# Performance work log

Measured on AMD Instinct MI355X. Metric: run time of the kernel, lower is better.

The kernel has to match this reference:

```python
import jax, jax.numpy as jnp
import numpy as np

N, E, H, G = 20000, 320000, 256, 128
FN, FE, OUT = 64, 16, 10
EPS_GEN = 1e-7
EPS_BN = 1e-5
EPS_IN = 1e-5


def _lstm_cell_c(x, W, b):
    # torch LSTMCell with zero (h0, c0); only cell state c' is used:
    # c' = sigmoid(i) * tanh(g).  W: [4H, F], gate order i, f, g, o.
    z = x @ W.T + b
    i, f, g, o = jnp.split(z, 4, axis=1)
    return jax.nn.sigmoid(i) * jnp.tanh(g)


def _segment_softmax(scores, seg, num):
    m = jax.ops.segment_max(scores, seg, num_segments=num)
    m = jnp.where(jnp.isfinite(m), m, 0.0)
    e = jnp.exp(scores - m[seg])
    s = jax.ops.segment_sum(e, seg, num_segments=num)
    return e / (s[seg] + 1e-16)


def _gen_conv(x, src, dst, edge_attr, t, w1, b1, gamma, beta, w2, b2):
    # GENConv (aggr='softmax', t learnable scalar, eps=1e-7, 2-layer MLP)
    msg = jax.nn.relu(x[src] + edge_attr) + EPS_GEN          # [E, H]
    alpha = _segment_softmax(msg * t, dst, N)                 # [E, H]
    aggr = jax.ops.segment_sum(alpha * msg, dst, num_segments=N)  # [N, H]
    h = x + aggr
    h = h @ w1.T + b1                                         # [N, 2H]
    # BatchNorm1d in eval mode (running_mean=0, running_var=1)
    h = h / jnp.sqrt(1.0 + EPS_BN) * gamma + beta
    h = jax.nn.relu(h)
    return h @ w2.T + b2                                      # [N, H]


def _instance_norm(x, batch):
    ones = jnp.ones((x.shape[0],), x.dtype)
    cnt = jnp.maximum(jax.ops.segment_sum(ones, batch, num_segments=G), 1.0)[:, None]
    mean = jax.ops.segment_sum(x, batch, num_segments=G) / cnt
    var = jax.ops.segment_sum(x * x, batch, num_segments=G) / cnt - mean ** 2
    return (x - mean[batch]) / jnp.sqrt(var[batch] + EPS_IN)


def setup_inputs() -> dict:
    key = jax.random.key(0)
    ks = jax.random.split(key, 24)

    def glorot(k, shape):
        lim = 1.0 / np.sqrt(shape[-1])
        return jax.random.uniform(k, shape, jnp.float32, -lim, lim)

    inp = {
        "x": jax.random.normal(ks[0], (N, FN), jnp.float32),
        "edge_index": jax.random.randint(ks[1], (2, E), 0, N),
        "edge_attr": jax.random.normal(ks[2], (E, FE), jnp.float32),
        "batch": jnp.sort(jax.random.randint(ks[3], (N,), 0, G)),
        # LSTMCell embeddings
        "node_W": glorot(ks[4], (4 * H, FN)),
        "node_b": glorot(ks[5], (4 * H,)),
        "edge_W": glorot(ks[6], (4 * H, FE)),
        "edge_b": glorot(ks[7], (4 * H,)),
        # GENConv 1
        "t1": jnp.float32(1.0),
        "g1_w1": glorot(ks[8], (2 * H, H)),
        "g1_b1": glorot(ks[9], (2 * H,)),
        "g1_gamma": jnp.ones((2 * H,), jnp.float32),
        "g1_beta": jnp.zeros((2 * H,), jnp.float32),
        "g1_w2": glorot(ks[10], (H, 2 * H)),
        "g1_b2": glorot(ks[11], (H,)),
        # GENConv 2
        "t2": jnp.float32(1.0),
        "g2_w1": glorot(ks[12], (2 * H, H)),
        "g2_b1": glorot(ks[13], (2 * H,)),
        "g2_gamma": jnp.ones((2 * H,), jnp.float32),
        "g2_beta": jnp.zeros((2 * H,), jnp.float32),
        "g2_w2": glorot(ks[14], (H, 2 * H)),
        "g2_b2": glorot(ks[15], (H,)),
        # output Linear
        "lin_w": glorot(ks[16], (OUT, H)),
        "lin_b": glorot(ks[17], (OUT,)),
    }
    return inp


def reference(x, edge_index, edge_attr, batch,
              node_W, node_b, edge_W, edge_b,
              t1, g1_w1, g1_b1, g1_gamma, g1_beta, g1_w2, g1_b2,
              t2, g2_w1, g2_b1, g2_gamma, g2_beta, g2_w2, g2_b2,
              lin_w, lin_b):
    src, dst = edge_index[0], edge_index[1]
    h = _lstm_cell_c(x, node_W, node_b)            # [N, H]
    ea = _lstm_cell_c(edge_attr, edge_W, edge_b)   # [E, H]
    h = jax.nn.relu(_gen_conv(h, src, dst, ea, t1, g1_w1, g1_b1, g1_gamma, g1_beta, g1_w2, g1_b2))
    h = _instance_norm(h, batch)
    h = jax.nn.relu(_gen_conv(h, src, dst, ea, t2, g2_w1, g2_b1, g2_gamma, g2_beta, g2_w2, g2_b2))
    h = _instance_norm(h, batch)
    pooled = jax.ops.segment_max(h, batch, num_segments=G)  # [G, H]
    pooled = jnp.where(jnp.isfinite(pooled), pooled, 0.0)
    # dropout is identity in eval mode
    out = pooled @ lin_w.T + lin_b
    return jax.nn.sigmoid(out)
```

## Files before the change

### kernel.cpp

```cpp
#include <hip/hip_runtime.h>
#include <math.h>

#define N_NODES 20000
#define N_EDGES 320000
#define HH      256
#define GG      128
#define FN      64
#define FE      16

__device__ __forceinline__ float fast_rcp(float x) {
    return __builtin_amdgcn_rcpf(x);
}
__device__ __forceinline__ float fast_sigmoid(float x) {
    return fast_rcp(1.f + __expf(-x));
}
__device__ __forceinline__ float sig_tanh(float zi, float zg) {
    float u = __expf(-zi);
    float v = __expf(2.f * zg);
    return (v - 1.f) * fast_rcp((1.f + u) * (v + 1.f));
}

__global__ void hist_k(const int* __restrict__ dst, int* __restrict__ cnt) {
    int e = blockIdx.x * blockDim.x + threadIdx.x;
    if (e < N_EDGES) atomicAdd(&cnt[dst[e]], 1);
}

__global__ __launch_bounds__(256) void scan1_k(const int* __restrict__ cnt,
                                               int* __restrict__ ex,
                                               int* __restrict__ bsum) {
    int b = blockIdx.x, t = threadIdx.x;
    int i = b * 256 + t;
    int v = (i < N_NODES) ? cnt[i] : 0;
    int lane = t & 63, w = t >> 6;
    int incl = v;
#pragma unroll
    for (int off = 1; off < 64; off <<= 1) {
        int u = __shfl_up(incl, off);
        if (lane >= off) incl += u;
    }
    __shared__ int wsum[4];
    if (lane == 63) wsum[w] = incl;
    __syncthreads();
    int woff = 0;
#pragma unroll
    for (int j = 0; j < 4; ++j)
        if (j < w) woff += wsum[j];
    if (i < N_NODES) ex[i] = woff + incl - v;
    if (t == 255) bsum[b] = woff + incl;
}

__global__ __launch_bounds__(128) void scan2_k(int* __restrict__ bsum, int nb) {
    int t = threadIdx.x;
    int v = (t < nb) ? bsum[t] : 0;
    int lane = t & 63, w = t >> 6;
    int incl = v;
#pragma unroll
    for (int off = 1; off < 64; off <<= 1) {
        int u = __shfl_up(incl, off);
        if (lane >= off) incl += u;
    }
    __shared__ int wsum[2];
    if (lane == 63) wsum[w] = incl;
    __syncthreads();
    int woff = (w == 1) ? wsum[0] : 0;
    if (t < nb) bsum[t] = woff + incl - v;
}

__global__ __launch_bounds__(256) void scan3_k(const int* __restrict__ cnt,
                                               const int* __restrict__ bsum,
                                               int* __restrict__ rowst,
                                               int* __restrict__ cursor) {
    int b = blockIdx.x, t = threadIdx.x;
    int i = b * 256 + t;
    if (i < N_NODES) {
        int v = rowst[i] + bsum[b];
        rowst[i] = v;
        cursor[i] = v;
        if (i == N_NODES - 1) rowst[N_NODES] = v + cnt[i];
    }
}

__global__ void scatter_k(const int* __restrict__ src,
                          const int* __restrict__ dst,
                          const float* __restrict__ eattr,
                          int* __restrict__ cursor, int* __restrict__ srcs,
                          float* __restrict__ eattrs) {
    int e = blockIdx.x * blockDim.x + threadIdx.x;
    if (e < N_EDGES) {
        int pos = atomicAdd(&cursor[dst[e]], 1);
        srcs[pos] = src[e];
        const float4* a = (const float4*)(eattr + (size_t)e * FE);
        float4* o = (float4*)(eattrs + (size_t)pos * FE);
        o[0] = a[0];
        o[1] = a[1];
        o[2] = a[2];
        o[3] = a[3];
    }
}

__global__ void repack_k(const float* __restrict__ W, const float* __restrict__ b,
                         float* __restrict__ W2, float* __restrict__ b2) {
    int idx = blockIdx.x * blockDim.x + threadIdx.x;
    if (idx < 512 * 64) {
        int r = idx >> 6, k = idx & 63;
        int c = r >> 1;
        int rs = (r & 1) ? (512 + c) : c;
        W2[idx] = W[rs * 64 + k];
    } else if (idx < 512 * 64 + 512) {
        int r = idx - 512 * 64;
        int c = r >> 1;
        int rs = (r & 1) ? (512 + c) : c;
        b2[r] = b[rs];
    }
}

#define NPB 8
__global__ __launch_bounds__(256, 4) void genconv_edge_k(
    const float* __restrict__ hin, const float* __restrict__ eattrs,
    const int* __restrict__ srcs, const int* __restrict__ rowst,
    const float* __restrict__ eW, const float* __restrict__ eb,
    const float* __restrict__ tptr, float* __restrict__ aout) {
    int tid = threadIdx.x;
    float wi[16], wg[16];
    const float4* Wi4 = (const float4*)(eW + (size_t)tid * FE);
    const float4* Wg4 = (const float4*)(eW + (size_t)(512 + tid) * FE);
#pragma unroll
    for (int q = 0; q < 4; ++q) {
        float4 a = Wi4[q], b = Wg4[q];
        wi[q * 4 + 0] = a.x; wi[q * 4 + 1] = a.y;
        wi[q * 4 + 2] = a.z; wi[q * 4 + 3] = a.w;
        wg[q * 4 + 0] = b.x; wg[q * 4 + 1] = b.y;
        wg[q * 4 + 2] = b.z; wg[q * 4 + 3] = b.w;
    }
    float bi = eb[tid], bg = eb[512 + tid];
    float tscale = tptr[0];
    int n0 = blockIdx.x * NPB;
    for (int u = 0; u < NPB; ++u) {
        int n = n0 + u;
        if (n >= N_NODES) break;
        int s0 = rowst[n], s1 = rowst[n + 1];
        float hself = hin[(size_t)n * HH + tid];
        float accE0 = 0.f, accWE0 = 0.f, accE1 = 0.f, accWE1 = 0.f;
        int j = s0;
        for (; j + 1 < s1; j += 2) {
            int sn0 = srcs[j], sn1 = srcs[j + 1];
            const float4* ap0 = (const float4*)(eattrs + (size_t)j * FE);
            const float4* ap1 = (const float4*)(eattrs + (size_t)(j + 1) * FE);
            float4 a0 = ap0[0], a1 = ap0[1], a2 = ap0[2], a3 = ap0[3];
            float4 c0 = ap1[0], c1 = ap1[1], c2 = ap1[2], c3 = ap1[3];
            float h0v = hin[(size_t)sn0 * HH + tid];
            float h1v = hin[(size_t)sn1 * HH + tid];
            float av[16] = {a0.x, a0.y, a0.z, a0.w, a1.x, a1.y, a1.z, a1.w,
                            a2.x, a2.y, a2.z, a2.w, a3.x, a3.y, a3.z, a3.w};
            float cv[16] = {c0.x, c0.y, c0.z, c0.w, c1.x, c1.y, c1.z, c1.w,
                            c2.x, c2.y, c2.z, c2.w, c3.x, c3.y, c3.z, c3.w};
            float zi0 = bi, zg0 = bg, zi1 = bi, zg1 = bg;
#pragma unroll
            for (int k = 0; k < FE; ++k) {
                zi0 += wi[k] * av[k];
                zg0 += wg[k] * av[k];
                zi1 += wi[k] * cv[k];
                zg1 += wg[k] * cv[k];
            }
            float ea0 = sig_tanh(zi0, zg0);
            float ea1 = sig_tanh(zi1, zg1);
            float m0 = fmaxf(h0v + ea0, 0.f) + 1e-7f;
            float m1 = fmaxf(h1v + ea1, 0.f) + 1e-7f;
            float p0 = __expf(tscale * m0);
            float p1 = __expf(tscale * m1);
            accE0 += p0;
            accWE0 += p0 * m0;
            accE1 += p1;
            accWE1 += p1 * m1;
        }
        if (j < s1) {
            int sn = srcs[j];
            const float4* ap = (const float4*)(eattrs + (size_t)j * FE);
            float4 a0 = ap[0], a1 = ap[1], a2 = ap[2], a3 = ap[3];
            float hv = hin[(size_t)sn * HH + tid];
            float av[16] = {a0.x, a0.y, a0.z, a0.w, a1.x, a1.y, a1.z, a1.w,
                            a2.x, a2.y, a2.z, a2.w, a3.x, a3.y, a3.z, a3.w};
            float zi = bi, zg = bg;
#pragma unroll
            for (int k = 0; k < FE; ++k) {
                zi += wi[k] * av[k];
                zg += wg[k] * av[k];
            }
            float eav = sig_tanh(zi, zg);
            float m0 = fmaxf(hv + eav, 0.f) + 1e-7f;
            float p0 = __expf(tscale * m0);
            accE0 += p0;
            accWE0 += p0 * m0;
        }
        float accE = accE0 + accE1, accWE = accWE0 + accWE1;
        aout[(size_t)n * HH + tid] = hself + accWE / (accE + 1e-16f);
    }
}

#define TM 128
#define TN 128
#define KB 16
__global__ __launch_bounds__(256, 2) void gemm_nt_k(
    const float* __restrict__ A, const float* __restrict__ B,
    const float* __restrict__ bias, const float* __restrict__ gamma,
    const float* __restrict__ beta, float* __restrict__ C, int M, int NN,
    int K, int mode) {
    __shared__ float As[KB][TM + 4];
    __shared__ float Bs[KB][TN + 4];
    int tid = threadIdx.x;
    int row0 = blockIdx.x * TM, col0 = blockIdx.y * TN;
    int tx = tid & 15, ty = tid >> 4;
    int lr = tid >> 2;
    int lc = (tid & 3) * 4;
    float4 va[2], vb[2];
#pragma unroll
    for (int h = 0; h < 2; ++h) {
        int r = lr + h * 64;
        int gr = row0 + r;
        va[h] = (gr < M) ? *(const float4*)&A[(size_t)gr * K + lc]
                         : make_float4(0.f, 0.f, 0.f, 0.f);
        vb[h] = *(const float4*)&B[(size_t)(col0 + r) * K + lc];
    }
    float acc[8][8] = {{0.f}};
    for (int k0 = 0; k0 < K; k0 += KB) {
#pragma unroll
        for (int h = 0; h < 2; ++h) {
            int r = lr + h * 64;
            As[lc + 0][r] = va[h].x;
            As[lc + 1][r] = va[h].y;
            As[lc + 2][r] = va[h].z;
            As[lc + 3][r] = va[h].w;
            Bs[lc + 0][r] = vb[h].x;
            Bs[lc + 1][r] = vb[h].y;
            Bs[lc + 2][r] = vb[h].z;
            Bs[lc + 3][r] = vb[h].w;
        }
        __syncthreads();
        int k1 = k0 + KB;
        if (k1 < K) {
#pragma unroll
            for (int h = 0; h < 2; ++h) {
                int r = lr + h * 64;
                int gr = row0 + r;
                va[h] = (gr < M)
                            ? *(const float4*)&A[(size_t)gr * K + k1 + lc]
                            : make_float4(0.f, 0.f, 0.f, 0.f);
                vb[h] = *(const float4*)&B[(size_t)(col0 + r) * K + k1 + lc];
            }
        }
#pragma unroll
        for (int k = 0; k < KB; ++k) {
            float4 a0 = *(const float4*)&As[k][ty * 4];
            float4 a1 = *(const float4*)&As[k][64 + ty * 4];
            float4 b0 = *(const float4*)&Bs[k][tx * 4];
            float4 b1 = *(const float4*)&Bs[k][64 + tx * 4];
            float av[8] = {a0.x, a0.y, a0.z, a0.w, a1.x, a1.y, a1.z, a1.w};
            float bv[8] = {b0.x, b0.y, b0.z, b0.w, b1.x, b1.y, b1.z, b1.w};
#pragma unroll
            for (int i = 0; i < 8; ++i)
#pragma unroll
                for (int j = 0; j < 8; ++j) acc[i][j] += av[i] * bv[j];
        }
        __syncthreads();
    }
    const float bn_rs = rsqrtf(1.f + 1e-5f);
#pragma unroll
    for (int gj = 0; gj < 2; ++gj) {
        int nb = col0 + gj * 64 + tx * 4;
        float bs[4], sc[4], sh[4];
#pragma unroll
        for (int j = 0; j < 4; ++j) {
            bs[j] = bias[nb + j];
            if (mode == 0) {
                sc[j] = gamma[nb + j] * bn_rs;
                sh[j] = beta[nb + j];
            }
        }
#pragma unroll
        for (int gi = 0; gi < 2; ++gi) {
#pragma unroll
            for (int i2 = 0; i2 < 4; ++i2) {
                int m = row0 + gi * 64 + ty * 4 + i2;
                if (m >= M) continue;
                int i = gi * 4 + i2;
                float y[4];
#pragma unroll
                for (int j = 0; j < 4; ++j) {
                    float v = acc[i][gj * 4 + j] + bs[j];
                    if (mode == 0) v = v * sc[j] + sh[j];
                    if (mode == 0 || mode == 1) v = fmaxf(v, 0.f);
                    y[j] = v;
                }
                if (mode == 3) {
                    float2 o;
                    o.x = sig_tanh(y[0], y[1]);
                    o.y = sig_tanh(y[2], y[3]);
                    *(float2*)&C[(size_t)m * (NN / 2) + nb / 2] = o;
                } else {
                    float4 o = {y[0], y[1], y[2], y[3]};
                    *(float4*)&C[(size_t)m * NN + nb] = o;
                }
            }
        }
    }
}

__device__ __forceinline__ int lowerb(const int* a, int n, int key) {
    int lo = 0, hi = n;
    while (lo < hi) {
        int mid = (lo + hi) >> 1;
        if (a[mid] < key) lo = mid + 1;
        else hi = mid;
    }
    return lo;
}

__global__ __launch_bounds__(256) void inst_norm_k(
    const float* __restrict__ x, const int* __restrict__ batch,
    float* __restrict__ y) {
    __shared__ int sS, sE;
    int g = blockIdx.x, t = threadIdx.x;
    if (t == 0) {
        sS = lowerb(batch, N_NODES, g);
        sE = lowerb(batch, N_NODES, g + 1);
    }
    __syncthreads();
    int s = sS, e = sE;
    float sum = 0.f, ss = 0.f;
    for (int n = s; n < e; ++n) {
        float v = x[(size_t)n * HH + t];
        sum += v;
        ss += v * v;
    }
    float c = (float)((e - s) > 0 ? (e - s) : 1);
    float mean = sum / c;
    float var = ss / c - mean * mean;
    float inv = rsqrtf(var + 1e-5f);
    for (int n = s; n < e; ++n) {
        float v = x[(size_t)n * HH + t];
        y[(size_t)n * HH + t] = (v - mean) * inv;
    }
}

__global__ __launch_bounds__(256) void inpool_k(
    const float* __restrict__ x, const int* __restrict__ batch,
    const float* __restrict__ lw, const float* __restrict__ lb,
    float* __restrict__ out) {
    __shared__ float pooled[HH];
    __shared__ int sS, sE;
    int g = blockIdx.x, t = threadIdx.x;
    if (t == 0) {
        sS = lowerb(batch, N_NODES, g);
        sE = lowerb(batch, N_NODES, g + 1);
    }
    __syncthreads();
    int s = sS, e = sE;
    float sum = 0.f, ss = 0.f;
    for (int n = s; n < e; ++n) {
        float v = x[(size_t)n * HH + t];
        sum += v;
        ss += v * v;
    }
    float c = (float)((e - s) > 0 ? (e - s) : 1);
    float mean = sum / c;
    float var = ss / c - mean * mean;
    float inv = rsqrtf(var + 1e-5f);
    float m = -3.0e38f;
    for (int n = s; n < e; ++n) {
        float v = (x[(size_t)n * HH + t] - mean) * inv;
        m = fmaxf(m, v);
    }
    pooled[t] = (e > s) ? m : 0.f;
    __syncthreads();
    if (t < 10) {
        float acc = lb[t];
        for (int k = 0; k < HH; ++k) acc += pooled[k] * lw[t * HH + k];
        out[g * 10 + t] = fast_sigmoid(acc);
    }
}

extern "C" void kernel_launch(void* const* d_in, const int* in_sizes, int n_in,
                              void* d_out, int out_size, void* d_ws,
                              size_t ws_size, hipStream_t stream) {
    const float* x      = (const float*)d_in[0];
    const int*   ei     = (const int*)d_in[1];
    const float* eattr  = (const float*)d_in[2];
    const int*   batch  = (const int*)d_in[3];
    const float* nodeW  = (const float*)d_in[4];
    const float* nodeb  = (const float*)d_in[5];
    const float* edgeW  = (const float*)d_in[6];
    const float* edgeb  = (const float*)d_in[7];
    const float* t1     = (const float*)d_in[8];
    const float* g1w1   = (const float*)d_in[9];
    const float* g1b1   = (const float*)d_in[10];
    const float* g1g    = (const float*)d_in[11];
    const float* g1be   = (const float*)d_in[12];
    const float* g1w2   = (const float*)d_in[13];
    const float* g1b2   = (const float*)d_in[14];
    const float* t2     = (const float*)d_in[15];
    const float* g2w1   = (const float*)d_in[16];
    const float* g2b1   = (const float*)d_in[17];
    const float* g2g    = (const float*)d_in[18];
    const float* g2be   = (const float*)d_in[19];
    const float* g2w2   = (const float*)d_in[20];
    const float* g2b2   = (const float*)d_in[21];
    const float* linw   = (const float*)d_in[22];
    const float* linb   = (const float*)d_in[23];
    float* out = (float*)d_out;

    const int* srcA = ei;
    const int* dstA = ei + N_EDGES;

    float* F0 = (float*)d_ws;
    float* F1 = F0 + (size_t)N_NODES * HH;
    float* F2 = F1 + (size_t)N_NODES * HH;
    float* W2 = F2 + (size_t)N_NODES * 2 * HH;
    float* b2 = W2 + 512 * 64;
    float* eattrs = b2 + 512;
    int* cnt    = (int*)(eattrs + (size_t)N_EDGES * FE);
    int* cursor = cnt + N_NODES;
    int* rowst  = cursor + N_NODES;
    int* srcs   = rowst + N_NODES + 1;
    int* bsum   = srcs + N_EDGES;

    const int NSCB = (N_NODES + 255) / 256;

    hipMemsetAsync(cnt, 0, N_NODES * sizeof(int), stream);
    hist_k<<<(N_EDGES + 255) / 256, 256, 0, stream>>>(dstA, cnt);
    scan1_k<<<NSCB, 256, 0, stream>>>(cnt, rowst, bsum);
    scan2_k<<<1, 128, 0, stream>>>(bsum, NSCB);
    scan3_k<<<NSCB, 256, 0, stream>>>(cnt, bsum, rowst, cursor);
    scatter_k<<<(N_EDGES + 255) / 256, 256, 0, stream>>>(srcA, dstA, eattr,
                                                         cursor, srcs, eattrs);

    repack_k<<<(512 * 64 + 512 + 255) / 256, 256, 0, stream>>>(nodeW, nodeb,
                                                               W2, b2);
    dim3 gemm_grid1((N_NODES + TM - 1) / TM, 512 / TN);
    dim3 gemm_grid2((N_NODES + TM - 1) / TM, 256 / TN);
    gemm_nt_k<<<gemm_grid1, 256, 0, stream>>>(x, W2, b2, nullptr, nullptr, F0,
                                              N_NODES, 512, 64, 3);

    genconv_edge_k<<<(N_NODES + NPB - 1) / NPB, 256, 0, stream>>>(
        F0, eattrs, srcs, rowst, edgeW, edgeb, t1, F1);
    gemm_nt_k<<<gemm_grid1, 256, 0, stream>>>(F1, g1w1, g1b1, g1g, g1be, F2,
                                              N_NODES, 512, 256, 0);
    gemm_nt_k<<<gemm_grid2, 256, 0, stream>>>(F2, g1w2, g1b2, nullptr, nullptr,
                                              F1, N_NODES, 256, 512, 1);
    inst_norm_k<<<GG, 256, 0, stream>>>(F1, batch, F0);

    genconv_edge_k<<<(N_NODES + NPB - 1) / NPB, 256, 0, stream>>>(
        F0, eattrs, srcs, rowst, edgeW, edgeb, t2, F1);
    gemm_nt_k<<<gemm_grid1, 256, 0, stream>>>(F1, g2w1, g2b1, g2g, g2be, F2,
                                              N_NODES, 512, 256, 0);
    gemm_nt_k<<<gemm_grid2, 256, 0, stream>>>(F2, g2w2, g2b2, nullptr, nullptr,
                                              F1, N_NODES, 256, 512, 1);

    inpool_k<<<GG, 256, 0, stream>>>(F1, batch, linw, linb, out);
}
```

Before: 985.6 us.

## Precompute edge LSTM embeddings once in bf16 via GEMM, reuse in both convs

The edge LSTM embedding was recomputed inside each genconv edge kernel, a 16-wide dot product plus sig_tanh per edge per channel, and done twice. It is now materialized once by the tiled GEMM with a new bf16-output epilogue, and both conv passes read it in CSR order. This trades compute for memory traffic: a 320000x256 bf16 tensor (~164MB) is written once and read twice instead of 64B of edge attributes per edge. Dropping the weight registers also lets launch bounds rise to 8 blocks per SM, and bf16 storage adds rounding error to the edge embedding.

```diff
diff --git a/kernel.cpp b/kernel.cpp
--- a/kernel.cpp
+++ b/kernel.cpp
@@ -1,4 +1,5 @@
 #include <hip/hip_runtime.h>
+#include <hip/hip_bf16.h>
 #include <math.h>
 
 #define N_NODES 20000
@@ -99,15 +100,15 @@
 }
 
 __global__ void repack_k(const float* __restrict__ W, const float* __restrict__ b,
-                         float* __restrict__ W2, float* __restrict__ b2) {
+                         float* __restrict__ W2, float* __restrict__ b2, int K) {
     int idx = blockIdx.x * blockDim.x + threadIdx.x;
-    if (idx < 512 * 64) {
-        int r = idx >> 6, k = idx & 63;
+    if (idx < 512 * K) {
+        int r = idx / K, k = idx - r * K;
         int c = r >> 1;
         int rs = (r & 1) ? (512 + c) : c;
-        W2[idx] = W[rs * 64 + k];
-    } else if (idx < 512 * 64 + 512) {
-        int r = idx - 512 * 64;
+        W2[idx] = W[rs * K + k];
+    } else if (idx < 512 * K + 512) {
+        int r = idx - 512 * K;
         int c = r >> 1;
         int rs = (r & 1) ? (512 + c) : c;
         b2[r] = b[rs];
@@ -115,24 +116,11 @@
 }
 
 #define NPB 8
-__global__ __launch_bounds__(256, 4) void genconv_edge_k(
-    const float* __restrict__ hin, const float* __restrict__ eattrs,
+__global__ __launch_bounds__(256, 8) void genconv_edge_k(
+    const float* __restrict__ hin, const __hip_bfloat16* __restrict__ eacsr,
     const int* __restrict__ srcs, const int* __restrict__ rowst,
-    const float* __restrict__ eW, const float* __restrict__ eb,
     const float* __restrict__ tptr, float* __restrict__ aout) {
     int tid = threadIdx.x;
-    float wi[16], wg[16];
-    const float4* Wi4 = (const float4*)(eW + (size_t)tid * FE);
-    const float4* Wg4 = (const float4*)(eW + (size_t)(512 + tid) * FE);
-#pragma unroll
-    for (int q = 0; q < 4; ++q) {
-        float4 a = Wi4[q], b = Wg4[q];
-        wi[q * 4 + 0] = a.x; wi[q * 4 + 1] = a.y;
-        wi[q * 4 + 2] = a.z; wi[q * 4 + 3] = a.w;
-        wg[q * 4 + 0] = b.x; wg[q * 4 + 1] = b.y;
-        wg[q * 4 + 2] = b.z; wg[q * 4 + 3] = b.w;
-    }
-    float bi = eb[tid], bg = eb[512 + tid];
     float tscale = tptr[0];
     int n0 = blockIdx.x * NPB;
     for (int u = 0; u < NPB; ++u) {
@@ -144,26 +132,10 @@
         int j = s0;
         for (; j + 1 < s1; j += 2) {
             int sn0 = srcs[j], sn1 = srcs[j + 1];
-            const float4* ap0 = (const float4*)(eattrs + (size_t)j * FE);
-            const float4* ap1 = (const float4*)(eattrs + (size_t)(j + 1) * FE);
-            float4 a0 = ap0[0], a1 = ap0[1], a2 = ap0[2], a3 = ap0[3];
-            float4 c0 = ap1[0], c1 = ap1[1], c2 = ap1[2], c3 = ap1[3];
+            float ea0 = __bfloat162float(eacsr[(size_t)j * HH + tid]);
+            float ea1 = __bfloat162float(eacsr[(size_t)(j + 1) * HH + tid]);
             float h0v = hin[(size_t)sn0 * HH + tid];
             float h1v = hin[(size_t)sn1 * HH + tid];
-            float av[16] = {a0.x, a0.y, a0.z, a0.w, a1.x, a1.y, a1.z, a1.w,
-                            a2.x, a2.y, a2.z, a2.w, a3.x, a3.y, a3.z, a3.w};
-            float cv[16] = {c0.x, c0.y, c0.z, c0.w, c1.x, c1.y, c1.z, c1.w,
-                            c2.x, c2.y, c2.z, c2.w, c3.x, c3.y, c3.z, c3.w};
-            float zi0 = bi, zg0 = bg, zi1 = bi, zg1 = bg;
-#pragma unroll
-            for (int k = 0; k < FE; ++k) {
-                zi0 += wi[k] * av[k];
-                zg0 += wg[k] * av[k];
-                zi1 += wi[k] * cv[k];
-                zg1 += wg[k] * cv[k];
-            }
-            float ea0 = sig_tanh(zi0, zg0);
-            float ea1 = sig_tanh(zi1, zg1);
             float m0 = fmaxf(h0v + ea0, 0.f) + 1e-7f;
             float m1 = fmaxf(h1v + ea1, 0.f) + 1e-7f;
             float p0 = __expf(tscale * m0);
@@ -175,18 +147,8 @@
         }
         if (j < s1) {
             int sn = srcs[j];
-            const float4* ap = (const float4*)(eattrs + (size_t)j * FE);
-            float4 a0 = ap[0], a1 = ap[1], a2 = ap[2], a3 = ap[3];
+            float eav = __bfloat162float(eacsr[(size_t)j * HH + tid]);
             float hv = hin[(size_t)sn * HH + tid];
-            float av[16] = {a0.x, a0.y, a0.z, a0.w, a1.x, a1.y, a1.z, a1.w,
-                            a2.x, a2.y, a2.z, a2.w, a3.x, a3.y, a3.z, a3.w};
-            float zi = bi, zg = bg;
-#pragma unroll
-            for (int k = 0; k < FE; ++k) {
-                zi += wi[k] * av[k];
-                zg += wg[k] * av[k];
-            }
-            float eav = sig_tanh(zi, zg);
             float m0 = fmaxf(hv + eav, 0.f) + 1e-7f;
             float p0 = __expf(tscale * m0);
             accE0 += p0;
@@ -296,6 +258,12 @@
                     o.x = sig_tanh(y[0], y[1]);
                     o.y = sig_tanh(y[2], y[3]);
                     *(float2*)&C[(size_t)m * (NN / 2) + nb / 2] = o;
+                } else if (mode == 4) {
+                    __hip_bfloat162 o;
+                    o.x = __float2bfloat16(sig_tanh(y[0], y[1]));
+                    o.y = __float2bfloat16(sig_tanh(y[2], y[3]));
+                    *(__hip_bfloat162*)((__hip_bfloat16*)C +
+                                        (size_t)m * (NN / 2) + nb / 2) = o;
                 } else {
                     float4 o = {y[0], y[1], y[2], y[3]};
                     *(float4*)&C[(size_t)m * NN + nb] = o;
@@ -411,13 +379,17 @@
     const int* srcA = ei;
     const int* dstA = ei + N_EDGES;
 
-    float* F0 = (float*)d_ws;
-    float* F1 = F0 + (size_t)N_NODES * HH;
-    float* F2 = F1 + (size_t)N_NODES * HH;
-    float* W2 = F2 + (size_t)N_NODES * 2 * HH;
-    float* b2 = W2 + 512 * 64;
-    float* eattrs = b2 + 512;
-    int* cnt    = (int*)(eattrs + (size_t)N_EDGES * FE);
+    float* F0  = (float*)d_ws;
+    float* F1  = F0 + (size_t)N_NODES * HH;
+    float* F2  = F1 + (size_t)N_NODES * HH;
+    float* W2n = F2 + (size_t)N_NODES * 2 * HH;
+    float* b2n = W2n + 512 * 64;
+    float* W2e = b2n + 512;
+    float* b2e = W2e + 512 * 16;
+    float* eattrs = b2e + 512;
+    __hip_bfloat16* eacsr =
+        (__hip_bfloat16*)(eattrs + (size_t)N_EDGES * FE);
+    int* cnt    = (int*)(eacsr + (size_t)N_EDGES * HH);
     int* cursor = cnt + N_NODES;
     int* rowst  = cursor + N_NODES;
     int* srcs   = rowst + N_NODES + 1;
@@ -434,14 +406,20 @@
                                                          cursor, srcs, eattrs);
 
     repack_k<<<(512 * 64 + 512 + 255) / 256, 256, 0, stream>>>(nodeW, nodeb,
-                                                               W2, b2);
+                                                               W2n, b2n, 64);
+    repack_k<<<(512 * 16 + 512 + 255) / 256, 256, 0, stream>>>(edgeW, edgeb,
+                                                               W2e, b2e, 16);
+
     dim3 gemm_grid1((N_NODES + TM - 1) / TM, 512 / TN);
     dim3 gemm_grid2((N_NODES + TM - 1) / TM, 256 / TN);
-    gemm_nt_k<<<gemm_grid1, 256, 0, stream>>>(x, W2, b2, nullptr, nullptr, F0,
-                                              N_NODES, 512, 64, 3);
+
+    gemm_nt_k<<<gemm_grid1, 256, 0, stream>>>(x, W2n, b2n, nullptr, nullptr,
+                                              F0, N_NODES, 512, 64, 3);
+    gemm_nt_k<<<dim3(N_EDGES / TM, 512 / TN), 256, 0, stream>>>(
+        eattrs, W2e, b2e, nullptr, nullptr, (float*)eacsr, N_EDGES, 512, 16, 4);
 
     genconv_edge_k<<<(N_NODES + NPB - 1) / NPB, 256, 0, stream>>>(
-        F0, eattrs, srcs, rowst, edgeW, edgeb, t1, F1);
+        F0, eacsr, srcs, rowst, t1, F1);
     gemm_nt_k<<<gemm_grid1, 256, 0, stream>>>(F1, g1w1, g1b1, g1g, g1be, F2,
                                               N_NODES, 512, 256, 0);
     gemm_nt_k<<<gemm_grid2, 256, 0, stream>>>(F2, g1w2, g1b2, nullptr, nullptr,
@@ -449,7 +427,7 @@
     inst_norm_k<<<GG, 256, 0, stream>>>(F1, batch, F0);
 
     genconv_edge_k<<<(N_NODES + NPB - 1) / NPB, 256, 0, stream>>>(
-        F0, eattrs, srcs, rowst, edgeW, edgeb, t2, F1);
+        F0, eacsr, srcs, rowst, t2, F1);
     gemm_nt_k<<<gemm_grid1, 256, 0, stream>>>(F1, g2w1, g2b1, g2g, g2be, F2,
                                               N_NODES, 512, 256, 0);
     gemm_nt_k<<<gemm_grid2, 256, 0, stream>>>(F2, g2w2, g2b2, nullptr, nullptr,
```

New measurement: 978.7 us. About the same (-0.7%).
